# Kernel tuning notes

Hardware: AMD Instinct MI355X
Metric: run time of the kernel (lower is better)

The kernel has to match this reference:

```python
import jax, jax.numpy as jnp
import numpy as np

N, F, H, C, HX, E = 50000, 256, 128, 16, 64, 500000
TEMP = 1.0


def gcn_conv(x, src, dst, W, b, n):
    # PyG GCNConv: x @ W, add self-loops, sym-normalized scatter-sum src->dst
    xw = x @ W
    idx = jnp.arange(n)
    s = jnp.concatenate([src, idx])
    d = jnp.concatenate([dst, idx])
    deg = jax.ops.segment_sum(jnp.ones_like(s, dtype=xw.dtype), d, num_segments=n)
    dinv = jnp.where(deg > 0, jax.lax.rsqrt(deg), 0.0)
    norm = dinv[s] * dinv[d]
    out = jax.ops.segment_sum(xw[s] * norm[:, None], d, num_segments=n)
    return out + b


def setup_inputs() -> dict:
    key = jax.random.key(0)
    ks = jax.random.split(key, 16)
    x = jax.random.normal(ks[0], (N, F), jnp.float32)
    edge_index = jax.random.randint(ks[1], (2, E), 0, N)
    neg_edge_index = jax.random.randint(ks[2], (2, E), 0, N)
    y = jax.random.randint(ks[3], (N,), 0, C)
    train_mask = jax.random.uniform(ks[4], (N,)) < 0.5
    def lin(k, fi, fo):
        s = 1.0 / np.sqrt(fi)
        return jax.random.uniform(k, (fi, fo), jnp.float32, -s, s)
    W1 = lin(ks[5], F, H); b1 = jnp.zeros((H,), jnp.float32)
    W2 = lin(ks[6], H, C); b2 = jnp.zeros((C,), jnp.float32)
    Wx = lin(ks[7], F, HX); bx = jnp.zeros((HX,), jnp.float32)
    Wd = lin(ks[8], 2 * (HX + C), 1); bd = jnp.zeros((1,), jnp.float32)
    return dict(x=x, edge_index=edge_index, neg_edge_index=neg_edge_index, y=y,
                train_mask=train_mask, W1=W1, b1=b1, W2=W2, b2=b2,
                Wx=Wx, bx=bx, Wd=Wd, bd=bd)


def reference(x, edge_index, neg_edge_index, y, train_mask,
              W1, b1, W2, b2, Wx, bx, Wd, bd):
    n = x.shape[0]
    # GNN encoder p(y|x,G): 2-layer GCN (eval mode -> dropout identity)
    h = jax.nn.relu(gcn_conv(x, edge_index[0], edge_index[1], W1, b1, n))
    logits = gcn_conv(h, edge_index[0], edge_index[1], W2, b2, n) / TEMP
    y_log_prob = jax.nn.log_softmax(logits, axis=-1)
    y_prob = jnp.where(train_mask[:, None],
                       jax.nn.one_hot(y, logits.shape[-1], dtype=logits.dtype),
                       jnp.exp(y_log_prob))
    # node feature encoder
    xe = jax.nn.relu(x @ Wx + bx)
    def decode(ei):
        s, d = ei[0], ei[1]
        feat = jnp.concatenate([xe[s], xe[d], y_prob[s], y_prob[d]], axis=1)
        return feat @ Wd + bd
    e_pred_pos = decode(edge_index)
    e_pred_neg = decode(neg_edge_index)
    return e_pred_pos, e_pred_neg, y_log_prob
```

## Files before the change

### kernel.cpp

```cpp
#include <hip/hip_runtime.h>

typedef unsigned short ushort_t;
typedef __attribute__((ext_vector_type(8))) short short8;
typedef __attribute__((ext_vector_type(4))) float floatx4;

constexpr int F = 256, H = 128, C = 16, HX = 64;
constexpr int NBCOL = H + HX;

__device__ __forceinline__ ushort_t f2bf(float f) {
  unsigned u = __float_as_uint(f);
  u += 0x7fffu + ((u >> 16) & 1u);
  return (ushort_t)(u >> 16);
}
__device__ __forceinline__ float bflo(unsigned u) { return __uint_as_float(u << 16); }
__device__ __forceinline__ float bfhi(unsigned u) { return __uint_as_float(u & 0xffff0000u); }

__global__ void k_pre(const float* __restrict__ x, ushort_t* __restrict__ xb, int totalU,
                      const float* __restrict__ W1, const float* __restrict__ Wx,
                      ushort_t* __restrict__ WBt,
                      const int* __restrict__ dst, int* __restrict__ deg, int e,
                      int n, int nbx, int nbw) {
  int b = blockIdx.x;
  if (b < nbx) {
    int i = b * 256 + threadIdx.x;
    if (i >= totalU) return;
    int tile = i >> 9, rem = i & 511, j = rem >> 4, l15 = rem & 15;
    int row = tile * 16 + l15;
    ushort4 lo = make_ushort4(0, 0, 0, 0), hi = lo;
    if (row < n) {
      const float4* xp = (const float4*)(x + (size_t)row * F + j * 8);
      float4 a = xp[0], bb = xp[1];
      lo = make_ushort4(f2bf(a.x), f2bf(a.y), f2bf(a.z), f2bf(a.w));
      hi = make_ushort4(f2bf(bb.x), f2bf(bb.y), f2bf(bb.z), f2bf(bb.w));
    }
    ((ushort4*)xb)[2 * i] = lo;
    ((ushort4*)xb)[2 * i + 1] = hi;
  } else if (b < nbx + nbw) {
    int i = (b - nbx) * 256 + threadIdx.x;
    if (i >= NBCOL * F) return;
    int nn = i / F, k = i % F;
    float v = (nn < H) ? W1[k * H + nn] : Wx[k * HX + (nn - H)];
    WBt[nn * F + k] = f2bf(v);
  } else {
    int i = (b - nbx - nbw) * 256 + threadIdx.x;
    if (i < e) atomicAdd(&deg[dst[i]], 1);
  }
}

__global__ void k_scan_a(const int* __restrict__ deg, int* __restrict__ part, int n) {
  __shared__ int sm[256];
  int i = blockIdx.x * 256 + threadIdx.x;
  int v = (i < n) ? deg[i] : 0;
  sm[threadIdx.x] = v;
  __syncthreads();
  for (int s = 128; s > 0; s >>= 1) {
    if (threadIdx.x < s) sm[threadIdx.x] += sm[threadIdx.x + s];
    __syncthreads();
  }
  if (threadIdx.x == 0) part[blockIdx.x] = sm[0];
}

__global__ void k_scan_c(const int* __restrict__ deg, const int* __restrict__ part,
                         int* __restrict__ row_start, int* __restrict__ cursor,
                         float* __restrict__ dinv, int n, int e) {
  __shared__ int psm[256];
  __shared__ int wsum[4], woff[4];
  int c = blockIdx.x, t = threadIdx.x;
  psm[t] = (t < c) ? part[t] : 0;
  __syncthreads();
  for (int s = 128; s > 0; s >>= 1) {
    if (t < s) psm[t] += psm[t + s];
    __syncthreads();
  }
  int blockoff = psm[0];
  __syncthreads();

  int i = c * 256 + t;
  int lane = t & 63, wid = t >> 6;
  int v = (i < n) ? deg[i] : 0;
  int xs = v;
  for (int d = 1; d < 64; d <<= 1) {
    int u = __shfl_up(xs, d);
    if (lane >= d) xs += u;
  }
  if (lane == 63) wsum[wid] = xs;
  __syncthreads();
  if (t == 0) {
    int s = 0;
    for (int w = 0; w < 4; w++) { woff[w] = s; s += wsum[w]; }
  }
  __syncthreads();
  int excl = xs - v + woff[wid] + blockoff;
  if (i < n) {
    row_start[i] = excl;
    cursor[i] = excl;
    dinv[i] = rsqrtf((float)(v + 1));
  }
  if (i == 0) row_start[n] = e;
}

__global__ void k_fill(const int* __restrict__ src, const int* __restrict__ dst,
                       const float* __restrict__ dinv, int* __restrict__ cursor,
                       int2* __restrict__ csr8, int e) {
  int i = blockIdx.x * 256 + threadIdx.x;
  if (i < e) {
    int s = src[i];
    int p = atomicAdd(&cursor[dst[i]], 1);
    csr8[p] = make_int2(s, __float_as_int(dinv[s]));
  }
}

__global__ __launch_bounds__(256, 3) void k_gemm1(const ushort_t* __restrict__ xb,
                                                  const ushort_t* __restrict__ WBt,
                                                  const float* __restrict__ bx,
                                                  ushort_t* __restrict__ xw1,
                                                  float* __restrict__ xe,
                                                  int n, int ntiles) {
  int w = threadIdx.x >> 6, lane = threadIdx.x & 63;
  int q = lane >> 4, l15 = lane & 15;
  const short8* bb = (const short8*)WBt;
  short8 bfr[3][8];
#pragma unroll
  for (int t = 0; t < 3; t++)
#pragma unroll
    for (int kk = 0; kk < 8; kk++)
      bfr[t][kk] = bb[(size_t)(w * 48 + t * 16 + l15) * 32 + kk * 4 + q];

  float bxv[3];
#pragma unroll
  for (int t = 0; t < 3; t++) {
    int g = w * 48 + t * 16;
    bxv[t] = (g >= H) ? bx[g - H + l15] : 0.0f;
  }

  const short8* ab = (const short8*)xb;
  for (int tile = blockIdx.x; tile < ntiles; tile += gridDim.x) {
    const short8* atile = ab + (size_t)tile * 512;
    short8 a[8];
#pragma unroll
    for (int kk = 0; kk < 8; kk++) a[kk] = atile[kk * 64 + q * 16 + l15];

    floatx4 acc0 = (floatx4)(0.0f), acc1 = (floatx4)(0.0f), acc2 = (floatx4)(0.0f);
#pragma unroll
    for (int kk = 0; kk < 8; kk++) {
      acc0 = __builtin_amdgcn_mfma_f32_16x16x32_bf16(a[kk], bfr[0][kk], acc0, 0, 0, 0);
      acc1 = __builtin_amdgcn_mfma_f32_16x16x32_bf16(a[kk], bfr[1][kk], acc1, 0, 0, 0);
      acc2 = __builtin_amdgcn_mfma_f32_16x16x32_bf16(a[kk], bfr[2][kk], acc2, 0, 0, 0);
    }

    floatx4 accs[3] = {acc0, acc1, acc2};
    int rbase = tile * 16 + q * 4;
#pragma unroll
    for (int t = 0; t < 3; t++) {
      int g = w * 48 + t * 16;
#pragma unroll
      for (int r = 0; r < 4; r++) {
        int ro = rbase + r;
        if (ro < n) {
          if (g < H) {
            xw1[(size_t)ro * H + g + l15] = f2bf(accs[t][r]);
          } else {
            xe[(size_t)ro * HX + (g - H) + l15] = fmaxf(accs[t][r] + bxv[t], 0.0f);
          }
        }
      }
    }
  }
}

__global__ void k_agg1g2(const ushort_t* __restrict__ xw1, const int* __restrict__ row_start,
                         const int2* __restrict__ csr8, const float* __restrict__ dinv,
                         const float* __restrict__ b1, const float* __restrict__ W2,
                         float* __restrict__ hw2, int n) {
  __shared__ float hsm[4][128];
  int wid = threadIdx.x >> 6;
  int v = blockIdx.x * 4 + wid;
  if (v >= n) return;
  int lane = threadIdx.x & 63;
  int g = lane >> 5, li = lane & 31;
  float dv = dinv[v];
  int j0 = row_start[v], j1 = row_start[v + 1];
  float ax0 = 0.0f, ay0 = 0.0f, ax1 = 0.0f, ay1 = 0.0f;
  for (int j = j0; j < j1; j += 16) {
    int2 ee[8];
    uint2 rr[8];
#pragma unroll
    for (int u = 0; u < 8; u++) {
      int je = j + g * 8 + u;
      ee[u] = csr8[je < j1 ? je : j0];
    }
#pragma unroll
    for (int u = 0; u < 8; u++)
      rr[u] = ((const uint2*)(xw1 + (size_t)ee[u].x * H))[li];
#pragma unroll
    for (int u = 0; u < 8; u++) {
      float wu = (j + g * 8 + u < j1) ? __int_as_float(ee[u].y) : 0.0f;
      ax0 += wu * bflo(rr[u].x);
      ay0 += wu * bfhi(rr[u].x);
      ax1 += wu * bflo(rr[u].y);
      ay1 += wu * bfhi(rr[u].y);
    }
  }
  ax0 += __shfl_xor(ax0, 32); ay0 += __shfl_xor(ay0, 32);
  ax1 += __shfl_xor(ax1, 32); ay1 += __shfl_xor(ay1, 32);
  uint2 sv = ((const uint2*)(xw1 + (size_t)v * H))[li];
  ax0 += dv * bflo(sv.x); ay0 += dv * bfhi(sv.x);
  ax1 += dv * bflo(sv.y); ay1 += dv * bfhi(sv.y);
  int c4 = li * 4;
  float o0 = fmaxf(dv * ax0 + b1[c4], 0.0f);
  float o1 = fmaxf(dv * ay0 + b1[c4 + 1], 0.0f);
  float o2 = fmaxf(dv * ax1 + b1[c4 + 2], 0.0f);
  float o3 = fmaxf(dv * ay1 + b1[c4 + 3], 0.0f);
  if (g == 0) *(float4*)&hsm[wid][c4] = make_float4(o0, o1, o2, o3);

  int c = lane & 15, gg = lane >> 4;
  const float* hrow = hsm[wid];
  float p = 0.0f;
#pragma unroll
  for (int jj = 0; jj < 32; jj++)
    p += hrow[gg * 32 + jj] * W2[(gg * 32 + jj) * C + c];
  p += __shfl_xor(p, 16);
  p += __shfl_xor(p, 32);
  if (gg == 0) hw2[(size_t)v * C + c] = p;
}

__global__ void k_agg2ab(const float* __restrict__ hw2, const int* __restrict__ row_start,
                         const int2* __restrict__ csr8, const float* __restrict__ dinv,
                         const float* __restrict__ b2, const int* __restrict__ y,
                         const int* __restrict__ tmask, const float* __restrict__ xe,
                         const float* __restrict__ Wd, float* __restrict__ ylp_out,
                         float* __restrict__ Aarr, float* __restrict__ Barr, int n) {
  int idx = blockIdx.x * 256 + threadIdx.x;
  int node = idx >> 4, c = idx & 15;
  if (node >= n) return;
  float dv = dinv[node];
  float acc = dv * hw2[(size_t)node * C + c];
  int j0 = row_start[node], j1 = row_start[node + 1];
  for (int j = j0; j < j1; j += 8) {
    int2 ee[8];
    float rr[8];
#pragma unroll
    for (int u = 0; u < 8; u++) {
      int je = j + u;
      ee[u] = csr8[je < j1 ? je : j0];
    }
#pragma unroll
    for (int u = 0; u < 8; u++) rr[u] = hw2[(size_t)ee[u].x * C + c];
#pragma unroll
    for (int u = 0; u < 8; u++)
      acc += ((j + u < j1) ? __int_as_float(ee[u].y) : 0.0f) * rr[u];
  }
  float logit = dv * acc + b2[c];
  float m = logit;
  for (int o = 8; o > 0; o >>= 1) m = fmaxf(m, __shfl_xor(m, o, 16));
  float e = expf(logit - m);
  float s16 = e;
  for (int o = 8; o > 0; o >>= 1) s16 += __shfl_xor(s16, o, 16);
  float lp = (logit - m) - logf(s16);
  ylp_out[(size_t)node * C + c] = lp;
  float yp = tmask[node] ? ((y[node] == c) ? 1.0f : 0.0f) : (e / s16);

  float4 xv = *(const float4*)(xe + (size_t)node * HX + c * 4);
  float4 wa = *(const float4*)(Wd + c * 4);
  float4 wb = *(const float4*)(Wd + HX + c * 4);
  float pa = xv.x * wa.x + xv.y * wa.y + xv.z * wa.z + xv.w * wa.w + yp * Wd[2 * HX + c];
  float pb = xv.x * wb.x + xv.y * wb.y + xv.z * wb.z + xv.w * wb.w + yp * Wd[2 * HX + C + c];
  for (int o = 8; o > 0; o >>= 1) {
    pa += __shfl_xor(pa, o, 16);
    pb += __shfl_xor(pb, o, 16);
  }
  if (c == 0) { Aarr[node] = pa; Barr[node] = pb; }
}

__global__ void k_decode(const int* __restrict__ ei, const int* __restrict__ nei,
                         const float* __restrict__ Aarr, const float* __restrict__ Barr,
                         const float* __restrict__ bd, float* __restrict__ out, int e) {
  int i = blockIdx.x * 256 + threadIdx.x;
  if (i >= 2 * e) return;
  float b0 = bd[0];
  if (i < e) {
    int s = ei[i], d = ei[e + i];
    out[i] = Aarr[s] + Barr[d] + b0;
  } else {
    int j = i - e;
    int s = nei[j], d = nei[e + j];
    out[e + j] = Aarr[s] + Barr[d] + b0;
  }
}

extern "C" void kernel_launch(void* const* d_in, const int* in_sizes, int n_in,
                              void* d_out, int out_size, void* d_ws, size_t ws_size,
                              hipStream_t stream) {
  const float* x = (const float*)d_in[0];
  const int* ei = (const int*)d_in[1];
  const int* nei = (const int*)d_in[2];
  const int* y = (const int*)d_in[3];
  const int* tmask = (const int*)d_in[4];
  const float* W1 = (const float*)d_in[5];
  const float* b1 = (const float*)d_in[6];
  const float* W2 = (const float*)d_in[7];
  const float* b2 = (const float*)d_in[8];
  const float* Wx = (const float*)d_in[9];
  const float* bx = (const float*)d_in[10];
  const float* Wd = (const float*)d_in[11];
  const float* bd = (const float*)d_in[12];
  float* out = (float*)d_out;

  int n = in_sizes[3];
  int e = in_sizes[1] / 2;
  int ntiles = (n + 15) / 16;

  char* ws = (char*)d_ws;
  size_t off = 0;
  auto alloc = [&](size_t bytes) -> void* {
    void* p = ws + off;
    off += (bytes + 511) & ~(size_t)511;
    return p;
  };
  int* deg = (int*)alloc((size_t)n * 4);
  ushort_t* xb = (ushort_t*)alloc((size_t)ntiles * 16 * F * 2);
  ushort_t* WBt = (ushort_t*)alloc((size_t)NBCOL * F * 2);
  ushort_t* xw1 = (ushort_t*)alloc((size_t)n * H * 2);
  float* xe = (float*)alloc((size_t)n * HX * 4);
  float* hw2 = (float*)alloc((size_t)n * C * 4);
  float* dinv = (float*)alloc((size_t)n * 4);
  int* row_start = (int*)alloc((size_t)(n + 1) * 4);
  int* cursor = (int*)alloc((size_t)n * 4);
  int2* csr8 = (int2*)alloc((size_t)e * 8);
  int* part = (int*)alloc(1024 * 4);
  float* Aarr = (float*)alloc((size_t)n * 4);
  float* Barr = (float*)alloc((size_t)n * 4);

  const int* src = ei;
  const int* dst = ei + e;

  hipMemsetAsync(deg, 0, (size_t)n * 4, stream);

  int totalU = ntiles * 512;
  int nbx = (totalU + 255) / 256;
  int nbw = (NBCOL * F + 255) / 256;
  int nbe = (e + 255) / 256;
  k_pre<<<nbx + nbw + nbe, 256, 0, stream>>>(x, xb, totalU, W1, Wx, WBt, dst, deg, e,
                                             n, nbx, nbw);

  int nchunk = (n + 255) / 256;
  k_scan_a<<<nchunk, 256, 0, stream>>>(deg, part, n);
  k_scan_c<<<nchunk, 256, 0, stream>>>(deg, part, row_start, cursor, dinv, n, e);
  k_fill<<<(e + 255) / 256, 256, 0, stream>>>(src, dst, dinv, cursor, csr8, e);

  int ggrid = ntiles < 768 ? ntiles : 768;
  k_gemm1<<<ggrid, 256, 0, stream>>>(xb, WBt, bx, xw1, xe, n, ntiles);
  k_agg1g2<<<(n + 3) / 4, 256, 0, stream>>>(xw1, row_start, csr8, dinv, b1, W2, hw2, n);
  k_agg2ab<<<(n * 16 + 255) / 256, 256, 0, stream>>>(hw2, row_start, csr8, dinv, b2, y,
                                                     tmask, xe, Wd, out + (size_t)2 * e,
                                                     Aarr, Barr, n);
  k_decode<<<(2 * e + 255) / 256, 256, 0, stream>>>(ei, nei, Aarr, Barr, bd, out, e);
}
```

Baseline: 258.7 us.

## Pad CSR rows to multiples of 16 with self-loop entry, switch xw1 to fp16

Each CSR row is rounded up to a multiple of 16 entries. The first pad slot holds the self-loop (the node itself with weight dinv) and the remaining slots hold zero weight, filled by a new k_pad kernel. This removes the bounds checks and the separate self-loop term from both aggregation kernels, and the second aggregation now unrolls 16 entries per step. The intermediate xw1 is stored as fp16 instead of bf16, and fma is used throughout. In exchange, the CSR grows (about e+16n entries), padded edges still cost gathers, and an extra kernel launch is added.

```diff
diff --git a/kernel.cpp b/kernel.cpp
--- a/kernel.cpp
+++ b/kernel.cpp
@@ -1,4 +1,5 @@
 #include <hip/hip_runtime.h>
+#include <hip/hip_fp16.h>
 
 typedef unsigned short ushort_t;
 typedef __attribute__((ext_vector_type(8))) short short8;
@@ -12,8 +13,6 @@
   u += 0x7fffu + ((u >> 16) & 1u);
   return (ushort_t)(u >> 16);
 }
-__device__ __forceinline__ float bflo(unsigned u) { return __uint_as_float(u << 16); }
-__device__ __forceinline__ float bfhi(unsigned u) { return __uint_as_float(u & 0xffff0000u); }
 
 __global__ void k_pre(const float* __restrict__ x, ushort_t* __restrict__ xb, int totalU,
                       const float* __restrict__ W1, const float* __restrict__ Wx,
@@ -50,7 +49,7 @@
 __global__ void k_scan_a(const int* __restrict__ deg, int* __restrict__ part, int n) {
   __shared__ int sm[256];
   int i = blockIdx.x * 256 + threadIdx.x;
-  int v = (i < n) ? deg[i] : 0;
+  int v = (i < n) ? ((deg[i] + 16) & ~15) : 0;
   sm[threadIdx.x] = v;
   __syncthreads();
   for (int s = 128; s > 0; s >>= 1) {
@@ -77,7 +76,8 @@
 
   int i = c * 256 + t;
   int lane = t & 63, wid = t >> 6;
-  int v = (i < n) ? deg[i] : 0;
+  int praw = (i < n) ? deg[i] : 0;
+  int v = (i < n) ? ((praw + 16) & ~15) : 0;
   int xs = v;
   for (int d = 1; d < 64; d <<= 1) {
     int u = __shfl_up(xs, d);
@@ -94,9 +94,9 @@
   if (i < n) {
     row_start[i] = excl;
     cursor[i] = excl;
-    dinv[i] = rsqrtf((float)(v + 1));
-  }
-  if (i == 0) row_start[n] = e;
+    dinv[i] = rsqrtf((float)(praw + 1));
+    if (i == n - 1) row_start[n] = excl + v;
+  }
 }
 
 __global__ void k_fill(const int* __restrict__ src, const int* __restrict__ dst,
@@ -108,6 +108,16 @@
     int p = atomicAdd(&cursor[dst[i]], 1);
     csr8[p] = make_int2(s, __float_as_int(dinv[s]));
   }
+}
+
+__global__ void k_pad(const int* __restrict__ cursor, const int* __restrict__ row_start,
+                      const float* __restrict__ dinv, int2* __restrict__ csr8, int n) {
+  int i = blockIdx.x * 256 + threadIdx.x;
+  int v = i >> 4, t = i & 15;
+  if (v >= n) return;
+  int p = cursor[v] + t;
+  if (p < row_start[v + 1])
+    csr8[p] = make_int2(v, t == 0 ? __float_as_int(dinv[v]) : 0);
 }
 
 __global__ __launch_bounds__(256, 3) void k_gemm1(const ushort_t* __restrict__ xb,
@@ -158,7 +168,8 @@
         int ro = rbase + r;
         if (ro < n) {
           if (g < H) {
-            xw1[(size_t)ro * H + g + l15] = f2bf(accs[t][r]);
+            __half hv = __float2half(accs[t][r]);
+            xw1[(size_t)ro * H + g + l15] = *reinterpret_cast<ushort_t*>(&hv);
           } else {
             xe[(size_t)ro * HX + (g - H) + l15] = fmaxf(accs[t][r] + bxv[t], 0.0f);
           }
@@ -185,32 +196,29 @@
     int2 ee[8];
     uint2 rr[8];
 #pragma unroll
-    for (int u = 0; u < 8; u++) {
-      int je = j + g * 8 + u;
-      ee[u] = csr8[je < j1 ? je : j0];
-    }
+    for (int u = 0; u < 8; u++) ee[u] = csr8[j + g * 8 + u];
 #pragma unroll
     for (int u = 0; u < 8; u++)
       rr[u] = ((const uint2*)(xw1 + (size_t)ee[u].x * H))[li];
 #pragma unroll
     for (int u = 0; u < 8; u++) {
-      float wu = (j + g * 8 + u < j1) ? __int_as_float(ee[u].y) : 0.0f;
-      ax0 += wu * bflo(rr[u].x);
-      ay0 += wu * bfhi(rr[u].x);
-      ax1 += wu * bflo(rr[u].y);
-      ay1 += wu * bfhi(rr[u].y);
+      float wu = __int_as_float(ee[u].y);
+      __half2 p0 = *reinterpret_cast<__half2*>(&rr[u].x);
+      __half2 p1 = *reinterpret_cast<__half2*>(&rr[u].y);
+      ax0 = fmaf(wu, __low2float(p0), ax0);
+      ay0 = fmaf(wu, __high2float(p0), ay0);
+      ax1 = fmaf(wu, __low2float(p1), ax1);
+      ay1 = fmaf(wu, __high2float(p1), ay1);
     }
   }
   ax0 += __shfl_xor(ax0, 32); ay0 += __shfl_xor(ay0, 32);
   ax1 += __shfl_xor(ax1, 32); ay1 += __shfl_xor(ay1, 32);
-  uint2 sv = ((const uint2*)(xw1 + (size_t)v * H))[li];
-  ax0 += dv * bflo(sv.x); ay0 += dv * bfhi(sv.x);
-  ax1 += dv * bflo(sv.y); ay1 += dv * bfhi(sv.y);
   int c4 = li * 4;
-  float o0 = fmaxf(dv * ax0 + b1[c4], 0.0f);
-  float o1 = fmaxf(dv * ay0 + b1[c4 + 1], 0.0f);
-  float o2 = fmaxf(dv * ax1 + b1[c4 + 2], 0.0f);
-  float o3 = fmaxf(dv * ay1 + b1[c4 + 3], 0.0f);
+  float4 b4 = *(const float4*)(b1 + c4);
+  float o0 = fmaxf(fmaf(dv, ax0, b4.x), 0.0f);
+  float o1 = fmaxf(fmaf(dv, ay0, b4.y), 0.0f);
+  float o2 = fmaxf(fmaf(dv, ax1, b4.z), 0.0f);
+  float o3 = fmaxf(fmaf(dv, ay1, b4.w), 0.0f);
   if (g == 0) *(float4*)&hsm[wid][c4] = make_float4(o0, o1, o2, o3);
 
   int c = lane & 15, gg = lane >> 4;
@@ -234,23 +242,19 @@
   int node = idx >> 4, c = idx & 15;
   if (node >= n) return;
   float dv = dinv[node];
-  float acc = dv * hw2[(size_t)node * C + c];
+  float acc = 0.0f;
   int j0 = row_start[node], j1 = row_start[node + 1];
-  for (int j = j0; j < j1; j += 8) {
-    int2 ee[8];
-    float rr[8];
-#pragma unroll
-    for (int u = 0; u < 8; u++) {
-      int je = j + u;
-      ee[u] = csr8[je < j1 ? je : j0];
-    }
-#pragma unroll
-    for (int u = 0; u < 8; u++) rr[u] = hw2[(size_t)ee[u].x * C + c];
-#pragma unroll
-    for (int u = 0; u < 8; u++)
-      acc += ((j + u < j1) ? __int_as_float(ee[u].y) : 0.0f) * rr[u];
-  }
-  float logit = dv * acc + b2[c];
+  for (int j = j0; j < j1; j += 16) {
+    int2 ee[16];
+    float rr[16];
+#pragma unroll
+    for (int u = 0; u < 16; u++) ee[u] = csr8[j + u];
+#pragma unroll
+    for (int u = 0; u < 16; u++) rr[u] = hw2[(size_t)ee[u].x * C + c];
+#pragma unroll
+    for (int u = 0; u < 16; u++) acc = fmaf(__int_as_float(ee[u].y), rr[u], acc);
+  }
+  float logit = fmaf(dv, acc, b2[c]);
   float m = logit;
   for (int o = 8; o > 0; o >>= 1) m = fmaxf(m, __shfl_xor(m, o, 16));
   float e = expf(logit - m);
@@ -326,7 +330,7 @@
   float* dinv = (float*)alloc((size_t)n * 4);
   int* row_start = (int*)alloc((size_t)(n + 1) * 4);
   int* cursor = (int*)alloc((size_t)n * 4);
-  int2* csr8 = (int2*)alloc((size_t)e * 8);
+  int2* csr8 = (int2*)alloc(((size_t)e + 16 * (size_t)n) * 8);
   int* part = (int*)alloc(1024 * 4);
   float* Aarr = (float*)alloc((size_t)n * 4);
   float* Barr = (float*)alloc((size_t)n * 4);
@@ -347,6 +351,7 @@
   k_scan_a<<<nchunk, 256, 0, stream>>>(deg, part, n);
   k_scan_c<<<nchunk, 256, 0, stream>>>(deg, part, row_start, cursor, dinv, n, e);
   k_fill<<<(e + 255) / 256, 256, 0, stream>>>(src, dst, dinv, cursor, csr8, e);
+  k_pad<<<(n * 16 + 255) / 256, 256, 0, stream>>>(cursor, row_start, dinv, csr8, n);
 
   int ggrid = ntiles < 768 ? ntiles : 768;
   k_gemm1<<<ggrid, 256, 0, stream>>>(xb, WBt, bx, xw1, xe, n, ntiles);
```

Result: faster. 251.7 us (-2.7%).
